# Kernel tuning notes

Measured on AMD Instinct MI355X. Metric: run time of the kernel, lower is better.

Reference implementation:

```python
import jax, jax.numpy as jnp
import numpy as np

BATCH = 4096
DIM = 512
TEMP = 0.5

def setup_inputs() -> dict:
    key = jax.random.key(0)
    k1, k2 = jax.random.split(key)
    emb_i = jax.random.normal(k1, (BATCH, DIM), dtype=jnp.float32)
    emb_j = jax.random.normal(k2, (BATCH, DIM), dtype=jnp.float32)
    return {"emb_i": emb_i, "emb_j": emb_j}

def reference(emb_i, emb_j):
    n = emb_i.shape[0]
    # L2-normalize once (torch F.normalize uses eps=1e-12 clamp on norm)
    z_i = emb_i / jnp.maximum(jnp.linalg.norm(emb_i, axis=1, keepdims=True), 1e-12)
    z_j = emb_j / jnp.maximum(jnp.linalg.norm(emb_j, axis=1, keepdims=True), 1e-12)
    z = jnp.concatenate([z_i, z_j], axis=0)            # [2N, D]
    sim = jnp.einsum('nd,md->nm', z, z)                # cosine sim, single GEMM
    # positives: diag(sim, +N) and diag(sim, -N) == rowwise dot(z_i, z_j)
    pos_ij = jnp.sum(z_i * z_j, axis=1)                # [N]
    positives = jnp.concatenate([pos_ij, pos_ij], 0)   # [2N]
    exp_sim = jnp.exp(sim / TEMP)
    mask = 1.0 - jnp.eye(2 * n, dtype=sim.dtype)
    denom = jnp.sum(mask * exp_sim, axis=1)            # [2N]
    loss_partial = -(positives / TEMP - jnp.log(denom))
    return jnp.sum(loss_partial) / (2 * n)
```

## Files before the change

kernel.cpp:

```cpp
#include <hip/hip_runtime.h>
#include <hip/hip_bf16.h>

#define N_ROWS 4096
#define DIM 512
#define TWO_N 8192
#define NTILE 64
#define NTRI  (NTILE * (NTILE + 1) / 2)

typedef __bf16 bf16x8 __attribute__((ext_vector_type(8)));
typedef float  f32x4  __attribute__((ext_vector_type(4)));

__device__ inline unsigned short f2bf(float f) {
    unsigned int u = __float_as_uint(f);
    u += 0x7fffu + ((u >> 16) & 1u);
    return (unsigned short)(u >> 16);
}

__device__ inline void g2l16(const void* g, void* l) {
    __builtin_amdgcn_global_load_lds(
        (const __attribute__((address_space(1))) void*)g,
        (__attribute__((address_space(3))) void*)l,
        16, 0, 0);
}

__global__ void normalize_kernel(const float* __restrict__ ei,
                                 const float* __restrict__ ej,
                                 unsigned short* __restrict__ zb,
                                 float* __restrict__ pos,
                                 float* __restrict__ denom,
                                 float* __restrict__ out) {
    int r = blockIdx.x;
    int t = threadIdx.x;
    const float2 vi = ((const float2*)(ei + (size_t)r * DIM))[t];
    const float2 vj = ((const float2*)(ej + (size_t)r * DIM))[t];
    float si  = vi.x * vi.x + vi.y * vi.y;
    float sj  = vj.x * vj.x + vj.y * vj.y;
    float sij = vi.x * vj.x + vi.y * vj.y;

    for (int o = 32; o; o >>= 1) {
        si  += __shfl_down(si, o);
        sj  += __shfl_down(sj, o);
        sij += __shfl_down(sij, o);
    }
    __shared__ float red[3][4];
    int wave = t >> 6, lane = t & 63;
    if (lane == 0) { red[0][wave] = si; red[1][wave] = sj; red[2][wave] = sij; }
    __syncthreads();
    si  = red[0][0] + red[0][1] + red[0][2] + red[0][3];
    sj  = red[1][0] + red[1][1] + red[1][2] + red[1][3];
    sij = red[2][0] + red[2][1] + red[2][2] + red[2][3];

    float rni = 1.0f / fmaxf(sqrtf(si), 1e-12f);
    float rnj = 1.0f / fmaxf(sqrtf(sj), 1e-12f);
    if (t == 0) {
        pos[r] = sij * rni * rnj;
        denom[r] = 0.0f;
        denom[r + N_ROWS] = 0.0f;
        if (r == 0) out[0] = 0.0f;
    }
    ushort2 zi2 = make_ushort2(f2bf(vi.x * rni), f2bf(vi.y * rni));
    ushort2 zj2 = make_ushort2(f2bf(vj.x * rnj), f2bf(vj.y * rnj));
    ((ushort2*)(zb + (size_t)r * DIM))[t] = zi2;
    ((ushort2*)(zb + (size_t)(r + N_ROWS) * DIM))[t] = zj2;
}

__global__ __launch_bounds__(256) void gemm_exp_kernel(
        const unsigned short* __restrict__ zb,
        float* __restrict__ denom) {
    const int t = blockIdx.x;
    int by = (int)(0.5f * (2.0f * NTILE + 1.0f -
              sqrtf((2.0f * NTILE + 1.0f) * (2.0f * NTILE + 1.0f) - 8.0f * t)));
    while ((by + 1) * NTILE - ((by + 1) * by) / 2 <= t) ++by;
    while (by * NTILE - (by * (by - 1)) / 2 > t) --by;
    const int bx = by + (t - (by * NTILE - (by * (by - 1)) / 2));

    const int rb = by * 128;
    const int cb = bx * 128;
    const bool diag = (rb == cb);

    const int tid  = threadIdx.x;
    const int wave = tid >> 6;
    const int lane = tid & 63;
    const int quad = lane >> 4;
    const int m    = lane & 15;
    const int wm   = (wave >> 1) * 64;
    const int wn   = (wave & 1) * 64;
    const int sq   = quad ^ ((m >> 1) & 3);

    __shared__ __align__(16) unsigned short As[128 * 32];
    __shared__ __align__(16) unsigned short Bs[128 * 32];

    f32x4 acc[4][4];
    #pragma unroll
    for (int i = 0; i < 4; ++i)
        #pragma unroll
        for (int j = 0; j < 4; ++j)
            #pragma unroll
            for (int r = 0; r < 4; ++r) acc[i][j][r] = 0.0f;

    const int srow = lane >> 2;
    const int sk   = (((lane & 3) ^ ((lane >> 3) & 3)) * 8);

    for (int k0 = 0; k0 < DIM; k0 += 32) {
        __syncthreads();
        #pragma unroll
        for (int cc = 0; cc < 2; ++cc) {
            int c   = 2 * wave + cc;
            int row = c * 16 + srow;
            const unsigned short* ga = zb + (size_t)(rb + row) * DIM + k0 + sk;
            const unsigned short* gb = zb + (size_t)(cb + row) * DIM + k0 + sk;
            g2l16(ga, As + c * 512);
            g2l16(gb, Bs + c * 512);
        }
        __syncthreads();

        bf16x8 af[4], bfr[4];
        #pragma unroll
        for (int i = 0; i < 4; ++i)
            af[i] = *(const bf16x8*)(As + (wm + i * 16 + m) * 32 + sq * 8);
        #pragma unroll
        for (int j = 0; j < 4; ++j)
            bfr[j] = *(const bf16x8*)(Bs + (wn + j * 16 + m) * 32 + sq * 8);

        #pragma unroll
        for (int i = 0; i < 4; ++i)
            #pragma unroll
            for (int j = 0; j < 4; ++j)
                acc[i][j] = __builtin_amdgcn_mfma_f32_16x16x32_bf16(
                    af[i], bfr[j], acc[i][j], 0, 0, 0);
    }

    __syncthreads();
    float* rs = (float*)As;
    float* cs = rs + 128;
    if (tid < 128) { rs[tid] = 0.0f; cs[tid] = 0.0f; }
    __syncthreads();

    float colsum[4] = {0.0f, 0.0f, 0.0f, 0.0f};
    #pragma unroll
    for (int i = 0; i < 4; ++i) {
        #pragma unroll
        for (int r = 0; r < 4; ++r) {
            int lrow = wm + i * 16 + quad * 4 + r;
            int grow = rb + lrow;
            float s = 0.0f;
            #pragma unroll
            for (int j = 0; j < 4; ++j) {
                int gcol = cb + wn + j * 16 + m;
                float v  = __expf(2.0f * acc[i][j][r]);
                v = (grow == gcol) ? 0.0f : v;
                s += v;
                colsum[j] += v;
            }
            s += __shfl_xor(s, 1);
            s += __shfl_xor(s, 2);
            s += __shfl_xor(s, 4);
            s += __shfl_xor(s, 8);
            if (m == 0) atomicAdd(&rs[lrow], s);
        }
    }
    if (!diag) {
        #pragma unroll
        for (int j = 0; j < 4; ++j) {
            float s = colsum[j];
            s += __shfl_xor(s, 16);
            s += __shfl_xor(s, 32);
            if (quad == 0) atomicAdd(&cs[wn + j * 16 + m], s);
        }
    }
    __syncthreads();
    if (tid < 128) {
        atomicAdd(&denom[rb + tid], rs[tid]);
        if (!diag) atomicAdd(&denom[cb + tid], cs[tid]);
    }
}

__global__ void loss_kernel(const float* __restrict__ pos,
                            const float* __restrict__ denom,
                            float* __restrict__ out) {
    int r = blockIdx.x * 256 + threadIdx.x;
    float s = __logf(denom[r]) - 2.0f * pos[r & (N_ROWS - 1)];
    for (int o = 32; o; o >>= 1) s += __shfl_down(s, o);
    __shared__ float red[4];
    int t = threadIdx.x;
    if ((t & 63) == 0) red[t >> 6] = s;
    __syncthreads();
    if (t == 0)
        atomicAdd(out, (red[0] + red[1] + red[2] + red[3]) / (float)TWO_N);
}

extern "C" void kernel_launch(void* const* d_in, const int* in_sizes, int n_in,
                              void* d_out, int out_size, void* d_ws, size_t ws_size,
                              hipStream_t stream) {
    const float* ei = (const float*)d_in[0];
    const float* ej = (const float*)d_in[1];

    unsigned short* zb  = (unsigned short*)d_ws;
    float* pos   = (float*)((char*)d_ws + (size_t)TWO_N * DIM * sizeof(unsigned short));
    float* denom = pos + N_ROWS;
    float* out   = (float*)d_out;

    normalize_kernel<<<N_ROWS, 256, 0, stream>>>(ei, ej, zb, pos, denom, out);
    gemm_exp_kernel<<<NTRI, 256, 0, stream>>>(zb, denom);
    loss_kernel<<<TWO_N / 256, 256, 0, stream>>>(pos, denom, out);
}
```

Before: 123.2 us.

## Load GEMM fragments directly from global memory with register double-buffering

Drops LDS staging in the similarity GEMM. Each wave now loads its bf16 A/B fragments straight from global memory into registers, with a two-deep register prefetch across the fully unrolled K loop, which removes the per-step barriers and LDS traffic. In exchange, each wave re-reads data that other waves share, so global/L2 load volume rises and each wave issues uncoalesced 16-byte loads, one row per lane. Register pressure also goes up.

```diff
diff --git a/kernel.cpp b/kernel.cpp
--- a/kernel.cpp
+++ b/kernel.cpp
@@ -14,13 +14,6 @@
     unsigned int u = __float_as_uint(f);
     u += 0x7fffu + ((u >> 16) & 1u);
     return (unsigned short)(u >> 16);
-}
-
-__device__ inline void g2l16(const void* g, void* l) {
-    __builtin_amdgcn_global_load_lds(
-        (const __attribute__((address_space(1))) void*)g,
-        (__attribute__((address_space(3))) void*)l,
-        16, 0, 0);
 }
 
 __global__ void normalize_kernel(const float* __restrict__ ei,
@@ -85,10 +78,14 @@
     const int m    = lane & 15;
     const int wm   = (wave >> 1) * 64;
     const int wn   = (wave & 1) * 64;
-    const int sq   = quad ^ ((m >> 1) & 3);
 
-    __shared__ __align__(16) unsigned short As[128 * 32];
-    __shared__ __align__(16) unsigned short Bs[128 * 32];
+    const unsigned short* pa[4];
+    const unsigned short* pb[4];
+    #pragma unroll
+    for (int i = 0; i < 4; ++i) {
+        pa[i] = zb + (size_t)(rb + wm + i * 16 + m) * DIM + quad * 8;
+        pb[i] = zb + (size_t)(cb + wn + i * 16 + m) * DIM + quad * 8;
+    }
 
     f32x4 acc[4][4];
     #pragma unroll
@@ -98,41 +95,33 @@
             #pragma unroll
             for (int r = 0; r < 4; ++r) acc[i][j][r] = 0.0f;
 
-    const int srow = lane >> 2;
-    const int sk   = (((lane & 3) ^ ((lane >> 3) & 3)) * 8);
+    bf16x8 af[2][4], bf_[2][4];
+    #pragma unroll
+    for (int i = 0; i < 4; ++i) {
+        af[0][i]  = *(const bf16x8*)(pa[i]);
+        bf_[0][i] = *(const bf16x8*)(pb[i]);
+    }
 
-    for (int k0 = 0; k0 < DIM; k0 += 32) {
-        __syncthreads();
-        #pragma unroll
-        for (int cc = 0; cc < 2; ++cc) {
-            int c   = 2 * wave + cc;
-            int row = c * 16 + srow;
-            const unsigned short* ga = zb + (size_t)(rb + row) * DIM + k0 + sk;
-            const unsigned short* gb = zb + (size_t)(cb + row) * DIM + k0 + sk;
-            g2l16(ga, As + c * 512);
-            g2l16(gb, Bs + c * 512);
+    #pragma unroll
+    for (int c = 0; c < 16; ++c) {
+        const int cur = c & 1, nxt = cur ^ 1;
+        if (c < 15) {
+            #pragma unroll
+            for (int i = 0; i < 4; ++i) {
+                af[nxt][i]  = *(const bf16x8*)(pa[i] + (c + 1) * 32);
+                bf_[nxt][i] = *(const bf16x8*)(pb[i] + (c + 1) * 32);
+            }
         }
-        __syncthreads();
-
-        bf16x8 af[4], bfr[4];
-        #pragma unroll
-        for (int i = 0; i < 4; ++i)
-            af[i] = *(const bf16x8*)(As + (wm + i * 16 + m) * 32 + sq * 8);
-        #pragma unroll
-        for (int j = 0; j < 4; ++j)
-            bfr[j] = *(const bf16x8*)(Bs + (wn + j * 16 + m) * 32 + sq * 8);
-
         #pragma unroll
         for (int i = 0; i < 4; ++i)
             #pragma unroll
             for (int j = 0; j < 4; ++j)
                 acc[i][j] = __builtin_amdgcn_mfma_f32_16x16x32_bf16(
-                    af[i], bfr[j], acc[i][j], 0, 0, 0);
+                    af[cur][i], bf_[cur][j], acc[i][j], 0, 0, 0);
     }
 
-    __syncthreads();
-    float* rs = (float*)As;
-    float* cs = rs + 128;
+    __shared__ float rs[128];
+    __shared__ float cs[128];
     if (tid < 128) { rs[tid] = 0.0f; cs[tid] = 0.0f; }
     __syncthreads();
 
```

Measured after the change: 210.4 us. +70.7%, slower.

## Fuse loss reduction into GEMM via last-block counter and double K-step per sync

Applied to the files above, without the earlier changes.

The separate loss kernel is removed. The GEMM kernel now increments a global counter, and the last block to finish computes the log-denominator sum and writes the output. The K loop also loads two 32-wide K slices per barrier pair, which halves the number of synchronisations and doubles the LDS footprint. The cost is one extra global atomic and fence per block, and a serial tail where a single block reduces 8192 values.

```diff
diff --git a/kernel.cpp b/kernel.cpp
--- a/kernel.cpp
+++ b/kernel.cpp
@@ -28,6 +28,7 @@
                                  unsigned short* __restrict__ zb,
                                  float* __restrict__ pos,
                                  float* __restrict__ denom,
+                                 unsigned int* __restrict__ cnt,
                                  float* __restrict__ out) {
     int r = blockIdx.x;
     int t = threadIdx.x;
@@ -56,7 +57,7 @@
         pos[r] = sij * rni * rnj;
         denom[r] = 0.0f;
         denom[r + N_ROWS] = 0.0f;
-        if (r == 0) out[0] = 0.0f;
+        if (r == 0) { cnt[0] = 0u; out[0] = 0.0f; }
     }
     ushort2 zi2 = make_ushort2(f2bf(vi.x * rni), f2bf(vi.y * rni));
     ushort2 zj2 = make_ushort2(f2bf(vj.x * rnj), f2bf(vj.y * rnj));
@@ -66,7 +67,10 @@
 
 __global__ __launch_bounds__(256) void gemm_exp_kernel(
         const unsigned short* __restrict__ zb,
-        float* __restrict__ denom) {
+        const float* __restrict__ pos,
+        float* __restrict__ denom,
+        unsigned int* __restrict__ cnt,
+        float* __restrict__ out) {
     const int t = blockIdx.x;
     int by = (int)(0.5f * (2.0f * NTILE + 1.0f -
               sqrtf((2.0f * NTILE + 1.0f) * (2.0f * NTILE + 1.0f) - 8.0f * t)));
@@ -87,8 +91,10 @@
     const int wn   = (wave & 1) * 64;
     const int sq   = quad ^ ((m >> 1) & 3);
 
-    __shared__ __align__(16) unsigned short As[128 * 32];
-    __shared__ __align__(16) unsigned short Bs[128 * 32];
+    __shared__ __align__(16) unsigned short As[2][128 * 32];
+    __shared__ __align__(16) unsigned short Bs[2][128 * 32];
+    __shared__ float redl[4];
+    __shared__ bool amLast;
 
     f32x4 acc[4][4];
     #pragma unroll
@@ -101,33 +107,38 @@
     const int srow = lane >> 2;
     const int sk   = (((lane & 3) ^ ((lane >> 3) & 3)) * 8);
 
-    for (int k0 = 0; k0 < DIM; k0 += 32) {
+    for (int k0 = 0; k0 < DIM; k0 += 64) {
         __syncthreads();
         #pragma unroll
-        for (int cc = 0; cc < 2; ++cc) {
-            int c   = 2 * wave + cc;
-            int row = c * 16 + srow;
-            const unsigned short* ga = zb + (size_t)(rb + row) * DIM + k0 + sk;
-            const unsigned short* gb = zb + (size_t)(cb + row) * DIM + k0 + sk;
-            g2l16(ga, As + c * 512);
-            g2l16(gb, Bs + c * 512);
+        for (int h = 0; h < 2; ++h) {
+            #pragma unroll
+            for (int cc = 0; cc < 2; ++cc) {
+                int c   = 2 * wave + cc;
+                int row = c * 16 + srow;
+                int kof = k0 + h * 32 + sk;
+                g2l16(zb + (size_t)(rb + row) * DIM + kof, As[h] + c * 512);
+                g2l16(zb + (size_t)(cb + row) * DIM + kof, Bs[h] + c * 512);
+            }
         }
         __syncthreads();
 
-        bf16x8 af[4], bfr[4];
-        #pragma unroll
-        for (int i = 0; i < 4; ++i)
-            af[i] = *(const bf16x8*)(As + (wm + i * 16 + m) * 32 + sq * 8);
-        #pragma unroll
-        for (int j = 0; j < 4; ++j)
-            bfr[j] = *(const bf16x8*)(Bs + (wn + j * 16 + m) * 32 + sq * 8);
-
-        #pragma unroll
-        for (int i = 0; i < 4; ++i)
+        #pragma unroll
+        for (int h = 0; h < 2; ++h) {
+            bf16x8 af[4], bfr[4];
+            #pragma unroll
+            for (int i = 0; i < 4; ++i)
+                af[i] = *(const bf16x8*)(As[h] + (wm + i * 16 + m) * 32 + sq * 8);
             #pragma unroll
             for (int j = 0; j < 4; ++j)
-                acc[i][j] = __builtin_amdgcn_mfma_f32_16x16x32_bf16(
-                    af[i], bfr[j], acc[i][j], 0, 0, 0);
+                bfr[j] = *(const bf16x8*)(Bs[h] + (wn + j * 16 + m) * 32 + sq * 8);
+
+            #pragma unroll
+            for (int i = 0; i < 4; ++i)
+                #pragma unroll
+                for (int j = 0; j < 4; ++j)
+                    acc[i][j] = __builtin_amdgcn_mfma_f32_16x16x32_bf16(
+                        af[i], bfr[j], acc[i][j], 0, 0, 0);
+        }
     }
 
     __syncthreads();
@@ -173,20 +184,25 @@
         atomicAdd(&denom[rb + tid], rs[tid]);
         if (!diag) atomicAdd(&denom[cb + tid], cs[tid]);
     }
-}
-
-__global__ void loss_kernel(const float* __restrict__ pos,
-                            const float* __restrict__ denom,
-                            float* __restrict__ out) {
-    int r = blockIdx.x * 256 + threadIdx.x;
-    float s = __logf(denom[r]) - 2.0f * pos[r & (N_ROWS - 1)];
-    for (int o = 32; o; o >>= 1) s += __shfl_down(s, o);
-    __shared__ float red[4];
-    int t = threadIdx.x;
-    if ((t & 63) == 0) red[t >> 6] = s;
-    __syncthreads();
-    if (t == 0)
-        atomicAdd(out, (red[0] + red[1] + red[2] + red[3]) / (float)TWO_N);
+
+    __threadfence();
+    __syncthreads();
+    if (tid == 0) amLast = (atomicAdd(cnt, 1u) == NTRI - 1);
+    __syncthreads();
+    if (amLast) {
+        __threadfence();
+        float s = 0.0f;
+        for (int r = tid; r < TWO_N; r += 256) {
+            float d = __hip_atomic_load(&denom[r], __ATOMIC_RELAXED,
+                                        __HIP_MEMORY_SCOPE_AGENT);
+            s += __logf(d) - 2.0f * pos[r & (N_ROWS - 1)];
+        }
+        for (int o = 32; o; o >>= 1) s += __shfl_down(s, o);
+        if ((tid & 63) == 0) redl[tid >> 6] = s;
+        __syncthreads();
+        if (tid == 0)
+            out[0] = (redl[0] + redl[1] + redl[2] + redl[3]) / (float)TWO_N;
+    }
 }
 
 extern "C" void kernel_launch(void* const* d_in, const int* in_sizes, int n_in,
@@ -198,9 +214,9 @@
     unsigned short* zb  = (unsigned short*)d_ws;
     float* pos   = (float*)((char*)d_ws + (size_t)TWO_N * DIM * sizeof(unsigned short));
     float* denom = pos + N_ROWS;
+    unsigned int* cnt = (unsigned int*)(denom + TWO_N);
     float* out   = (float*)d_out;
 
-    normalize_kernel<<<N_ROWS, 256, 0, stream>>>(ei, ej, zb, pos, denom, out);
-    gemm_exp_kernel<<<NTRI, 256, 0, stream>>>(zb, denom);
-    loss_kernel<<<TWO_N / 256, 256, 0, stream>>>(pos, denom, out);
-}
+    normalize_kernel<<<N_ROWS, 256, 0, stream>>>(ei, ej, zb, pos, denom, cnt, out);
+    gemm_exp_kernel<<<NTRI, 256, 0, stream>>>(zb, pos, denom, cnt, out);
+}
```

Measured after the change: 239.7 us. 94.6% more time.
